# Kernel optimization log

Hardware: AMD Instinct MI355X
Metric: run time of the kernel (lower is better)

The kernel has to match this reference:

```python
import jax, jax.numpy as jnp
import numpy as np

HEADS = 8
DIM_HEAD = 64


def setup_inputs() -> dict:
    key = jax.random.key(0)
    ks = jax.random.split(key, 5)
    dim = 512
    dim_inner = HEADS * DIM_HEAD
    return {
        "fmap": jax.random.normal(ks[0], (8, dim, 32, 32), dtype=jnp.float32),
        "gamma": jnp.ones((dim,), dtype=jnp.float32),
        "wq": jax.random.normal(ks[1], (dim_inner, dim), dtype=jnp.float32) * 0.05,
        "wv": jax.random.normal(ks[2], (dim_inner, dim), dtype=jnp.float32) * 0.05,
        "null_kv": jax.random.normal(ks[3], (2, HEADS, DIM_HEAD), dtype=jnp.float32),
        "wo": jax.random.normal(ks[4], (dim, dim_inner), dtype=jnp.float32) * 0.05,
    }


def reference(fmap, gamma, wq, wv, null_kv, wo):
    b, c, H, W = fmap.shape
    h, d = HEADS, DIM_HEAD
    n = H * W
    scale = d ** (-0.5)

    # ChannelRMSNorm: F.normalize over channel dim * sqrt(dim) * gamma
    l2 = jnp.sqrt(jnp.sum(fmap * fmap, axis=1, keepdims=True))
    x = fmap / jnp.maximum(l2, 1e-12) * (c ** 0.5) * gamma[None, :, None, None]

    # 1x1 convs as channel matmuls -> [b, h, n, d]
    def proj(w):
        t = jnp.einsum('bcxy,oc->boxy', x, w)          # [b, h*d, H, W]
        return t.reshape(b, h, d, n).transpose(0, 1, 3, 2)  # [b, h, n, d]

    q = proj(wq)
    v = proj(wv)
    k = q  # dot_product=False -> to_k is None, k = q

    # prepend null kv token
    nk = jnp.broadcast_to(null_kv[0][None, :, None, :], (b, h, 1, d))
    nv = jnp.broadcast_to(null_kv[1][None, :, None, :], (b, h, 1, d))
    k = jnp.concatenate([nk, k], axis=2)  # [b, h, n+1, d]
    v = jnp.concatenate([nv, v], axis=2)

    # negative squared L2 distance score: -(|q|^2 + |k|^2 - 2 q.k)
    q_sq = jnp.sum(q * q, axis=-1)  # [b, h, n]
    k_sq = jnp.sum(k * k, axis=-1)  # [b, h, n+1]
    qk = jnp.einsum('bhid,bhjd->bhij', q, k)
    sim = -(q_sq[..., :, None] + k_sq[..., None, :] - 2.0 * qk) * scale

    attn = jax.nn.softmax(sim, axis=-1)
    out = jnp.einsum('bhij,bhjd->bhid', attn, v)  # [b, h, n, d]

    out = out.transpose(0, 1, 3, 2).reshape(b, h * d, H, W)
    return jnp.einsum('boxy,co->bcxy', out, wo)
```

## Files before the change

### kernel.cpp

```cpp
#include <hip/hip_runtime.h>
#include <hip/hip_bf16.h>

#define DEV static __device__ __forceinline__

typedef __bf16 bf16x8 __attribute__((ext_vector_type(8)));
typedef float f32x4 __attribute__((ext_vector_type(4)));
typedef float f32x16 __attribute__((ext_vector_type(16)));
typedef unsigned u32x4 __attribute__((ext_vector_type(4)));
typedef unsigned short u16x8 __attribute__((ext_vector_type(8)));
typedef unsigned short u16x4 __attribute__((ext_vector_type(4)));

DEV unsigned short f2bf(float f) {
  unsigned u = __builtin_bit_cast(unsigned, f);
  u += 0x7fffu + ((u >> 16) & 1u);
  return (unsigned short)(u >> 16);
}
DEV float bf2f(unsigned short s) {
  return __builtin_bit_cast(float, (unsigned)s << 16);
}
DEV f32x4 mfma16(bf16x8 a, bf16x8 b, f32x4 c) {
  return __builtin_amdgcn_mfma_f32_16x16x32_bf16(a, b, c, 0, 0, 0);
}
DEV f32x16 mfma32(bf16x8 a, bf16x8 b, f32x16 c) {
  return __builtin_amdgcn_mfma_f32_32x32x16_bf16(a, b, c, 0, 0, 0);
}
DEV bf16x8 ld8(const unsigned short* p) {
  return __builtin_bit_cast(bf16x8, *(const u16x8*)p);
}
DEV void gload16(const unsigned short* g, unsigned short* l) {
  auto* g1 = reinterpret_cast<const __attribute__((address_space(1))) unsigned int*>(
      reinterpret_cast<uintptr_t>(g));
  auto* l3 = reinterpret_cast<__attribute__((address_space(3))) unsigned int*>(
      reinterpret_cast<uintptr_t>(l));
  __builtin_amdgcn_global_load_lds(g1, l3, 16, 0, 0);
}

__global__ __launch_bounds__(256) void prep_k(const float* __restrict__ fmap,
                                              const float* __restrict__ gamma,
                                              const float* __restrict__ wq,
                                              const float* __restrict__ wv,
                                              const float* __restrict__ wo,
                                              unsigned short* __restrict__ xt,
                                              unsigned short* __restrict__ wqb,
                                              unsigned short* __restrict__ wvb,
                                              unsigned short* __restrict__ wob) {
  int bid = blockIdx.x, tid = threadIdx.x;
  if (bid >= 256) {
    int t4 = bid - 256;
    int g = t4 >> 5;
    const float* src = (g == 0) ? wq : (g == 1) ? wv : wo;
    unsigned short* dst = (g == 0) ? wqb : (g == 1) ? wvb : wob;
    int base = (t4 & 31) * 1024 + tid;
    const float4* s = (const float4*)src;
#pragma unroll
    for (int i = 0; i < 4; ++i) {
      int idx = base + i * 256;
      float4 a = s[idx * 2], b = s[idx * 2 + 1];
      u16x8 o;
      o[0] = f2bf(a.x); o[1] = f2bf(a.y); o[2] = f2bf(a.z); o[3] = f2bf(a.w);
      o[4] = f2bf(b.x); o[5] = f2bf(b.y); o[6] = f2bf(b.z); o[7] = f2bf(b.w);
      ((u16x8*)dst)[idx] = o;
    }
    return;
  }
  __shared__ float slab[512][33];
  __shared__ float red[8][32];
  __shared__ float rn_l[32];
  __shared__ float gl[512];
  int b = bid >> 5, n0 = (bid & 31) * 32;
  gl[tid] = gamma[tid];
  gl[tid + 256] = gamma[tid + 256];
  int n_l = tid & 31, cg = tid >> 5;
  const float* p = fmap + ((size_t)(b * 512 + cg * 64)) * 1024 + n0 + n_l;
  float s = 0.f;
#pragma unroll 8
  for (int i = 0; i < 64; ++i) {
    float v = p[i * 1024];
    slab[cg * 64 + i][n_l] = v;
    s += v * v;
  }
  red[cg][n_l] = s;
  __syncthreads();
  if (tid < 32) {
    float ts = 0.f;
#pragma unroll
    for (int k = 0; k < 8; ++k) ts += red[k][tid];
    rn_l[tid] = 22.62741699796952f / fmaxf(sqrtf(ts), 1e-12f);
  }
  __syncthreads();
  int nn = tid >> 3, cc = tid & 7;
  float sc = rn_l[nn];
#pragma unroll
  for (int c0 = 0; c0 < 512; c0 += 64) {
    u16x8 o;
#pragma unroll
    for (int e = 0; e < 8; ++e) {
      int c = c0 + cc * 8 + e;
      o[e] = f2bf(slab[c][nn] * sc * gl[c]);
    }
    *(u16x8*)(xt + ((size_t)(b * 1024 + n0 + nn)) * 512 + c0 + cc * 8) = o;
  }
}

__global__ __launch_bounds__(512) void gemm_qv_k(const unsigned short* __restrict__ A,
                                                 const unsigned short* __restrict__ wqb,
                                                 const unsigned short* __restrict__ wvb,
                                                 const float* __restrict__ nkv,
                                                 unsigned short* __restrict__ QF,
                                                 unsigned short* __restrict__ VF,
                                                 float* __restrict__ qsqs,
                                                 float* __restrict__ p0g) {
  __shared__ unsigned short a_lds[128 * 64];
  __shared__ unsigned short bq_lds[128 * 64];
  __shared__ unsigned short bv_lds[128 * 64];
  int tid = threadIdx.x, lane = tid & 63, wid = tid >> 6;
  int isV = wid >> 2, gw = wid & 3;
  int wr = gw >> 1, wc = gw & 1;
  int m0 = blockIdx.y * 128, n0 = blockIdx.x * 128;
  int srow = (lane >> 3);
  int scol = ((lane & 7) ^ ((lane >> 3) & 7)) * 8;
  f32x4 acc[4][4] = {};
  for (int kt = 0; kt < 512; kt += 64) {
    int il0 = wid * 2;
#pragma unroll
    for (int i = 0; i < 2; ++i) {
      int il = il0 + i;
      gload16(A + (size_t)(m0 + il * 8 + srow) * 512 + kt + scol, &a_lds[il * 512]);
      gload16(wqb + (size_t)(n0 + il * 8 + srow) * 512 + kt + scol, &bq_lds[il * 512]);
      gload16(wvb + (size_t)(n0 + il * 8 + srow) * 512 + kt + scol, &bv_lds[il * 512]);
    }
    __syncthreads();
    const unsigned short* bl = isV ? bv_lds : bq_lds;
#pragma unroll
    for (int ks = 0; ks < 2; ++ks) {
      int c = ks * 4 + (lane >> 4);
      int cs = (c ^ (lane & 7)) * 8;
      bf16x8 af[4], bfr[4];
#pragma unroll
      for (int rt = 0; rt < 4; ++rt)
        af[rt] = ld8(&a_lds[(wr * 64 + rt * 16 + (lane & 15)) * 64 + cs]);
#pragma unroll
      for (int ct = 0; ct < 4; ++ct)
        bfr[ct] = ld8(&bl[(wc * 64 + ct * 16 + (lane & 15)) * 64 + cs]);
#pragma unroll
      for (int rt = 0; rt < 4; ++rt)
#pragma unroll
        for (int ct = 0; ct < 4; ++ct)
          acc[rt][ct] = mfma16(af[rt], bfr[ct], acc[rt][ct]);
    }
    __syncthreads();
  }
  if (!isV) {
    const float COEF = 0.18033688011112042f;
    int head = blockIdx.x * 2 + wc;
    const float* nk = nkv + head * 64;
    float nk_own[4], nks = 0.f;
#pragma unroll
    for (int ct = 0; ct < 4; ++ct) {
      nk_own[ct] = nk[ct * 16 + (lane & 15)];
      nks += nk_own[ct] * nk_own[ct];
    }
    nks += __shfl_xor(nks, 1); nks += __shfl_xor(nks, 2);
    nks += __shfl_xor(nks, 4); nks += __shfl_xor(nks, 8);
#pragma unroll
    for (int rt = 0; rt < 4; ++rt)
#pragma unroll
      for (int r = 0; r < 4; ++r) {
        float qs = 0.f, dot = 0.f;
        unsigned short qr[4];
#pragma unroll
        for (int ct = 0; ct < 4; ++ct) {
          unsigned short us = f2bf(acc[rt][ct][r]);
          qr[ct] = us;
          float v = bf2f(us);
          qs += v * v;
          dot += v * nk_own[ct];
        }
        int n = m0 + wr * 64 + rt * 16 + (lane >> 4) * 4 + r;
        int bb = n >> 10, nl = n & 1023;
        int bh = bb * 8 + head;
        size_t fidx = (size_t)(bh * 32 + (nl >> 5)) * 2048 + (nl & 31) * 16 + (lane & 15);
#pragma unroll
        for (int ct = 0; ct < 4; ++ct) QF[fidx + ct * 512] = qr[ct];
        qs += __shfl_xor(qs, 1); qs += __shfl_xor(qs, 2);
        qs += __shfl_xor(qs, 4); qs += __shfl_xor(qs, 8);
        dot += __shfl_xor(dot, 1); dot += __shfl_xor(dot, 2);
        dot += __shfl_xor(dot, 4); dot += __shfl_xor(dot, 8);
        if ((lane & 15) == 0) {
          qsqs[bh * 1024 + nl] = qs * COEF;
          p0g[bh * 1024 + nl] = __builtin_amdgcn_exp2f((2.f * dot - nks) * COEF);
        }
      }
  } else {
#pragma unroll
    for (int rt = 0; rt < 4; ++rt)
#pragma unroll
      for (int ct = 0; ct < 4; ++ct) {
        int nb = m0 + wr * 64 + rt * 16 + (lane >> 4) * 4;
        int o = n0 + wc * 64 + ct * 16 + (lane & 15);
        int b = nb >> 10, j = nb & 1023;
        int h = o >> 6, d = o & 63;
        int bh = b * 8 + h;
        size_t idx = (size_t)(bh * 32 + (j >> 5)) * 2048 + ((j >> 4) & 1) * 1024 + (d >> 5) * 512 +
                     (d & 31) * 16 + (j & 15);
        u16x4 pk;
#pragma unroll
        for (int r = 0; r < 4; ++r) pk[r] = f2bf(acc[rt][ct][r]);
        *(u16x4*)(VF + idx) = pk;
      }
  }
}

__global__ __launch_bounds__(256) void gemm_o_k(const unsigned short* __restrict__ A,
                                                const unsigned short* __restrict__ Bt,
                                                float* __restrict__ Cp) {
  __shared__ unsigned short a_lds[64 * 64];
  __shared__ unsigned short b_lds[128 * 64];
  int bid = blockIdx.x;
  int y = (bid >> 3) & 7;
  int x = (bid & 7) + ((bid >> 6) << 3);
  int m0 = y * 64, n0 = x * 128;
  int tid = threadIdx.x, lane = tid & 63, wid = tid >> 6;
  int wr = wid >> 1, wc = wid & 1;
  int srow = (lane >> 3);
  int scol = ((lane & 7) ^ ((lane >> 3) & 7)) * 8;
  f32x4 acc[2][4] = {};
  for (int kt = 0; kt < 512; kt += 64) {
#pragma unroll
    for (int i = 0; i < 2; ++i) {
      int il = wid * 2 + i;
      gload16(A + (size_t)(m0 + il * 8 + srow) * 512 + kt + scol, &a_lds[il * 512]);
    }
#pragma unroll
    for (int i = 0; i < 4; ++i) {
      int il = wid * 4 + i;
      gload16(Bt + (size_t)(n0 + il * 8 + srow) * 512 + kt + scol, &b_lds[il * 512]);
    }
    __syncthreads();
#pragma unroll
    for (int ks = 0; ks < 2; ++ks) {
      int c = ks * 4 + (lane >> 4);
      int cs = (c ^ (lane & 7)) * 8;
      bf16x8 af[2], bfr[4];
#pragma unroll
      for (int rt = 0; rt < 2; ++rt)
        af[rt] = ld8(&a_lds[(wr * 32 + rt * 16 + (lane & 15)) * 64 + cs]);
#pragma unroll
      for (int ct = 0; ct < 4; ++ct)
        bfr[ct] = ld8(&b_lds[(wc * 64 + ct * 16 + (lane & 15)) * 64 + cs]);
#pragma unroll
      for (int rt = 0; rt < 2; ++rt)
#pragma unroll
        for (int ct = 0; ct < 4; ++ct)
          acc[rt][ct] = mfma16(af[rt], bfr[ct], acc[rt][ct]);
    }
    __syncthreads();
  }
  int bb = n0 >> 10;
#pragma unroll
  for (int rt = 0; rt < 2; ++rt)
#pragma unroll
    for (int ct = 0; ct < 4; ++ct)
#pragma unroll
      for (int r = 0; r < 4; ++r) {
        int row = m0 + wr * 32 + rt * 16 + (lane >> 4) * 4 + r;
        int col = (n0 & 1023) + wc * 64 + ct * 16 + (lane & 15);
        Cp[((size_t)(bb * 512 + row)) * 1024 + col] = acc[rt][ct][r];
      }
}

__global__ __launch_bounds__(512) void attn_k(const unsigned short* __restrict__ QF,
                                              const unsigned short* __restrict__ VF,
                                              const float* __restrict__ qsqs,
                                              const float* __restrict__ p0g,
                                              const float* __restrict__ nkv,
                                              unsigned short* __restrict__ att) {
  const float C2 = 0.36067376022224085f;
  int bid = blockIdx.x;
  int s0 = bid >> 3;
  int bh = ((bid & 7) << 3) | (s0 & 7);
  int qt = s0 >> 3;
  int b = bh >> 3, h = bh & 7;
  int n0 = qt * 128;
  int tid = threadIdx.x, lane = tid & 63, wid = tid >> 6;
  int wq = wid & 3, jg = wid >> 2;
  int l31 = lane & 31, hi = lane >> 5;

  __shared__ float ob_l[32][4][64];
  __shared__ float dsb[4][32];
  __shared__ float p0_l[128];
  __shared__ float nv_l[64];
  __shared__ float dn_l[4][32];

  if (tid < 128) p0_l[tid] = p0g[bh * 1024 + n0 + tid];
  else if (tid < 192) nv_l[tid - 128] = nkv[512 + h * 64 + (tid - 128)];
  __syncthreads();

  bf16x8 qf[4];
  const unsigned short* qfp = QF + (size_t)(bh * 32 + qt * 4 + wq) * 2048 + l31 * 16 + hi * 8;
#pragma unroll
  for (int ks = 0; ks < 4; ++ks)
    qf[ks] = ld8(qfp + ks * 512);

  f32x16 oacc[2];
#pragma unroll
  for (int dh = 0; dh < 2; ++dh)
#pragma unroll
    for (int r = 0; r < 16; ++r) {
      int row = (r & 3) + 8 * (r >> 2) + 4 * hi;
      oacc[dh][r] = (jg == 0) ? p0_l[wq * 32 + row] * nv_l[dh * 32 + l31] : 0.f;
    }

  f32x4 dsum4 = {0.f, 0.f, 0.f, 0.f};
  const unsigned short* kbase = QF + (size_t)bh * 65536 + l31 * 16 + hi * 8;
  const unsigned short* vbase = VF + (size_t)bh * 65536 + l31 * 16 + hi * 8;
  const float* ksb = qsqs + bh * 1024 + 4 * hi;

  bf16x8 kfA[4], kfB[4], vfA[2][2], vfB[2][2];
  f32x4 ksqA[4], ksqB[4];

#define LOADT(S, JT)                                                        \
  {                                                                         \
    const unsigned short* kp_ = kbase + (JT) * 2048;                        \
    kf##S[0] = ld8(kp_);        kf##S[1] = ld8(kp_ + 512);                  \
    kf##S[2] = ld8(kp_ + 1024); kf##S[3] = ld8(kp_ + 1536);                 \
    const unsigned short* vp_ = vbase + (JT) * 2048;                        \
    vf##S[0][0] = ld8(vp_);        vf##S[0][1] = ld8(vp_ + 1024);           \
    vf##S[1][0] = ld8(vp_ + 512);  vf##S[1][1] = ld8(vp_ + 1536);           \
    const float* kq_ = ksb + (JT) * 32;                                     \
    ksq##S[0] = *(const f32x4*)(kq_);      ksq##S[1] = *(const f32x4*)(kq_ + 8);  \
    ksq##S[2] = *(const f32x4*)(kq_ + 16); ksq##S[3] = *(const f32x4*)(kq_ + 24); \
  }

#define COMPT(S)                                                            \
  {                                                                         \
    f32x16 sacc = {};                                                       \
    __builtin_amdgcn_s_setprio(1);                                          \
    sacc = mfma32(kf##S[0], qf[0], sacc);                                   \
    sacc = mfma32(kf##S[1], qf[1], sacc);                                   \
    sacc = mfma32(kf##S[2], qf[2], sacc);                                   \
    sacc = mfma32(kf##S[3], qf[3], sacc);                                   \
    __builtin_amdgcn_s_setprio(0);                                          \
    float p[16];                                                            \
    _Pragma("unroll")                                                       \
    for (int r = 0; r < 16; ++r) {                                          \
      p[r] = __builtin_amdgcn_exp2f(sacc[r] * C2 - ksq##S[r >> 2][r & 3]);  \
      dsum4[r & 3] += p[r];                                                 \
    }                                                                       \
    unsigned w[4][2];                                                       \
    _Pragma("unroll")                                                       \
    for (int m = 0; m < 4; ++m) {                                           \
      asm("v_cvt_pk_bf16_f32 %0, %1, %2" : "=v"(w[m][0]) : "v"(p[4 * m]), "v"(p[4 * m + 1]));     \
      asm("v_cvt_pk_bf16_f32 %0, %1, %2" : "=v"(w[m][1]) : "v"(p[4 * m + 2]), "v"(p[4 * m + 3])); \
    }                                                                       \
    __builtin_amdgcn_s_setprio(1);                                          \
    _Pragma("unroll")                                                       \
    for (int sj = 0; sj < 2; ++sj) {                                        \
      unsigned a0 = w[2 * sj][0], b0 = w[2 * sj + 1][0];                    \
      unsigned a1 = w[2 * sj][1], b1 = w[2 * sj + 1][1];                    \
      asm("v_permlane32_swap_b32 %0, %1" : "+v"(a0), "+v"(b0));             \
      asm("v_permlane32_swap_b32 %0, %1" : "+v"(a1), "+v"(b1));             \
      u32x4 pw; pw[0] = a0; pw[1] = a1; pw[2] = b0; pw[3] = b1;             \
      bf16x8 pa = __builtin_bit_cast(bf16x8, pw);                           \
      oacc[0] = mfma32(pa, vf##S[0][sj], oacc[0]);                          \
      oacc[1] = mfma32(pa, vf##S[1][sj], oacc[1]);                          \
    }                                                                       \
    __builtin_amdgcn_s_setprio(0);                                          \
  }

  int jb = jg * 16;
  LOADT(A, jb)
#pragma unroll 1
  for (int s = 0; s < 7; ++s) {
    LOADT(B, jb + 2 * s + 1)
    COMPT(A)
    LOADT(A, jb + 2 * s + 2)
    COMPT(B)
  }
  LOADT(B, jb + 15)
  COMPT(A)
  COMPT(B)

  float dsum = (dsum4[0] + dsum4[1]) + (dsum4[2] + dsum4[3]);
  dsum += __shfl_xor(dsum, 32);

  if (jg == 1) {
#pragma unroll
    for (int dh = 0; dh < 2; ++dh)
#pragma unroll
      for (int r = 0; r < 16; ++r)
        ob_l[dh * 16 + r][wq][lane] = oacc[dh][r];
    if (hi == 0) dsb[wq][l31] = dsum;
  }
  __syncthreads();
  if (jg == 0) {
#pragma unroll
    for (int dh = 0; dh < 2; ++dh)
#pragma unroll
      for (int r = 0; r < 16; ++r)
        oacc[dh][r] += ob_l[dh * 16 + r][wq][lane];
    dsum += dsb[wq][l31] + p0_l[wq * 32 + l31];
    float rden = 1.0f / dsum;
    if (hi == 0) dn_l[wq][l31] = rden;
  }
  __syncthreads();

  if (jg == 0) {
#pragma unroll
    for (int dh = 0; dh < 2; ++dh)
#pragma unroll
      for (int r = 0; r < 16; ++r) {
        int row = (r & 3) + 8 * (r >> 2) + 4 * hi;
        float o = oacc[dh][r] * dn_l[wq][row];
        att[((size_t)(b * 1024 + n0 + wq * 32 + row)) * 512 + h * 64 + dh * 32 + l31] = f2bf(o);
      }
  }
}

extern "C" void kernel_launch(void* const* d_in, const int* in_sizes, int n_in,
                              void* d_out, int out_size, void* d_ws, size_t ws_size,
                              hipStream_t stream) {
  const float* fmap = (const float*)d_in[0];
  const float* gamma = (const float*)d_in[1];
  const float* wq = (const float*)d_in[2];
  const float* wv = (const float*)d_in[3];
  const float* nkv = (const float*)d_in[4];
  const float* wo = (const float*)d_in[5];
  float* out = (float*)d_out;

  const size_t M4 = (size_t)8192 * 512;
  unsigned short* x_t = (unsigned short*)d_ws;
  unsigned short* QF  = x_t + M4;
  unsigned short* VF  = QF + M4;
  unsigned short* att = VF + M4;
  unsigned short* wqb = att + M4;
  unsigned short* wvb = wqb + (size_t)512 * 512;
  unsigned short* wob = wvb + (size_t)512 * 512;
  float* qsqs = (float*)(wob + (size_t)512 * 512);
  float* p0g  = qsqs + 65536;

  prep_k<<<352, 256, 0, stream>>>(fmap, gamma, wq, wv, wo, x_t, wqb, wvb, wob);
  gemm_qv_k<<<dim3(4, 64), 512, 0, stream>>>(x_t, wqb, wvb, nkv, QF, VF, qsqs, p0g);
  attn_k<<<512, 512, 0, stream>>>(QF, VF, qsqs, p0g, nkv, att);
  gemm_o_k<<<512, 256, 0, stream>>>(wob, att, out);
}
```

Baseline: 69.84 us.

## Double-buffer LDS tiles in projection GEMMs and split QK MFMA accumulator chains

Both the QV projection GEMM and the output GEMM now keep two LDS buffers, so the global-to-LDS loads for the next K tile are issued before computing on the current one. This is meant to hide global load latency behind the MFMA work, at the cost of twice the shared memory, which may lower occupancy. In the attention kernel, the four dependent QK MFMAs are split into two independent accumulators that are summed before the exp. This shortens the MFMA dependency chain at the cost of one extra add per element.

```diff
diff --git a/kernel.cpp b/kernel.cpp
--- a/kernel.cpp
+++ b/kernel.cpp
@@ -110,9 +110,9 @@
                                                  unsigned short* __restrict__ VF,
                                                  float* __restrict__ qsqs,
                                                  float* __restrict__ p0g) {
-  __shared__ unsigned short a_lds[128 * 64];
-  __shared__ unsigned short bq_lds[128 * 64];
-  __shared__ unsigned short bv_lds[128 * 64];
+  __shared__ unsigned short a_lds[2][128 * 64];
+  __shared__ unsigned short bq_lds[2][128 * 64];
+  __shared__ unsigned short bv_lds[2][128 * 64];
   int tid = threadIdx.x, lane = tid & 63, wid = tid >> 6;
   int isV = wid >> 2, gw = wid & 3;
   int wr = gw >> 1, wc = gw & 1;
@@ -120,17 +120,28 @@
   int srow = (lane >> 3);
   int scol = ((lane & 7) ^ ((lane >> 3) & 7)) * 8;
   f32x4 acc[4][4] = {};
-  for (int kt = 0; kt < 512; kt += 64) {
-    int il0 = wid * 2;
-#pragma unroll
-    for (int i = 0; i < 2; ++i) {
-      int il = il0 + i;
-      gload16(A + (size_t)(m0 + il * 8 + srow) * 512 + kt + scol, &a_lds[il * 512]);
-      gload16(wqb + (size_t)(n0 + il * 8 + srow) * 512 + kt + scol, &bq_lds[il * 512]);
-      gload16(wvb + (size_t)(n0 + il * 8 + srow) * 512 + kt + scol, &bv_lds[il * 512]);
-    }
-    __syncthreads();
-    const unsigned short* bl = isV ? bv_lds : bq_lds;
+
+#define QV_STAGE(BUF, KT)                                                          \
+  {                                                                                \
+    int il0 = wid * 2;                                                             \
+    _Pragma("unroll")                                                              \
+    for (int i = 0; i < 2; ++i) {                                                  \
+      int il = il0 + i;                                                            \
+      gload16(A + (size_t)(m0 + il * 8 + srow) * 512 + (KT) + scol, &a_lds[BUF][il * 512]);   \
+      gload16(wqb + (size_t)(n0 + il * 8 + srow) * 512 + (KT) + scol, &bq_lds[BUF][il * 512]); \
+      gload16(wvb + (size_t)(n0 + il * 8 + srow) * 512 + (KT) + scol, &bv_lds[BUF][il * 512]); \
+    }                                                                              \
+  }
+
+  QV_STAGE(0, 0)
+  asm volatile("s_waitcnt vmcnt(0)" ::: "memory");
+  __syncthreads();
+  int cur = 0;
+#pragma unroll 1
+  for (int t = 0; t < 8; ++t) {
+    if (t < 7) QV_STAGE(cur ^ 1, (t + 1) * 64)
+    const unsigned short* al = &a_lds[cur][0];
+    const unsigned short* bl = isV ? &bv_lds[cur][0] : &bq_lds[cur][0];
 #pragma unroll
     for (int ks = 0; ks < 2; ++ks) {
       int c = ks * 4 + (lane >> 4);
@@ -138,7 +149,7 @@
       bf16x8 af[4], bfr[4];
 #pragma unroll
       for (int rt = 0; rt < 4; ++rt)
-        af[rt] = ld8(&a_lds[(wr * 64 + rt * 16 + (lane & 15)) * 64 + cs]);
+        af[rt] = ld8(&al[(wr * 64 + rt * 16 + (lane & 15)) * 64 + cs]);
 #pragma unroll
       for (int ct = 0; ct < 4; ++ct)
         bfr[ct] = ld8(&bl[(wc * 64 + ct * 16 + (lane & 15)) * 64 + cs]);
@@ -148,7 +159,9 @@
         for (int ct = 0; ct < 4; ++ct)
           acc[rt][ct] = mfma16(af[rt], bfr[ct], acc[rt][ct]);
     }
+    asm volatile("s_waitcnt vmcnt(0)" ::: "memory");
     __syncthreads();
+    cur ^= 1;
   }
   if (!isV) {
     const float COEF = 0.18033688011112042f;
@@ -214,8 +227,8 @@
 __global__ __launch_bounds__(256) void gemm_o_k(const unsigned short* __restrict__ A,
                                                 const unsigned short* __restrict__ Bt,
                                                 float* __restrict__ Cp) {
-  __shared__ unsigned short a_lds[64 * 64];
-  __shared__ unsigned short b_lds[128 * 64];
+  __shared__ unsigned short a_lds[2][64 * 64];
+  __shared__ unsigned short b_lds[2][128 * 64];
   int bid = blockIdx.x;
   int y = (bid >> 3) & 7;
   int x = (bid & 7) + ((bid >> 6) << 3);
@@ -225,18 +238,30 @@
   int srow = (lane >> 3);
   int scol = ((lane & 7) ^ ((lane >> 3) & 7)) * 8;
   f32x4 acc[2][4] = {};
-  for (int kt = 0; kt < 512; kt += 64) {
-#pragma unroll
-    for (int i = 0; i < 2; ++i) {
-      int il = wid * 2 + i;
-      gload16(A + (size_t)(m0 + il * 8 + srow) * 512 + kt + scol, &a_lds[il * 512]);
-    }
-#pragma unroll
-    for (int i = 0; i < 4; ++i) {
-      int il = wid * 4 + i;
-      gload16(Bt + (size_t)(n0 + il * 8 + srow) * 512 + kt + scol, &b_lds[il * 512]);
-    }
-    __syncthreads();
+
+#define O_STAGE(BUF, KT)                                                           \
+  {                                                                                \
+    _Pragma("unroll")                                                              \
+    for (int i = 0; i < 2; ++i) {                                                  \
+      int il = wid * 2 + i;                                                        \
+      gload16(A + (size_t)(m0 + il * 8 + srow) * 512 + (KT) + scol, &a_lds[BUF][il * 512]);    \
+    }                                                                              \
+    _Pragma("unroll")                                                              \
+    for (int i = 0; i < 4; ++i) {                                                  \
+      int il = wid * 4 + i;                                                        \
+      gload16(Bt + (size_t)(n0 + il * 8 + srow) * 512 + (KT) + scol, &b_lds[BUF][il * 512]);   \
+    }                                                                              \
+  }
+
+  O_STAGE(0, 0)
+  asm volatile("s_waitcnt vmcnt(0)" ::: "memory");
+  __syncthreads();
+  int cur = 0;
+#pragma unroll 1
+  for (int t = 0; t < 8; ++t) {
+    if (t < 7) O_STAGE(cur ^ 1, (t + 1) * 64)
+    const unsigned short* al = &a_lds[cur][0];
+    const unsigned short* bl = &b_lds[cur][0];
 #pragma unroll
     for (int ks = 0; ks < 2; ++ks) {
       int c = ks * 4 + (lane >> 4);
@@ -244,17 +269,19 @@
       bf16x8 af[2], bfr[4];
 #pragma unroll
       for (int rt = 0; rt < 2; ++rt)
-        af[rt] = ld8(&a_lds[(wr * 32 + rt * 16 + (lane & 15)) * 64 + cs]);
+        af[rt] = ld8(&al[(wr * 32 + rt * 16 + (lane & 15)) * 64 + cs]);
 #pragma unroll
       for (int ct = 0; ct < 4; ++ct)
-        bfr[ct] = ld8(&b_lds[(wc * 64 + ct * 16 + (lane & 15)) * 64 + cs]);
+        bfr[ct] = ld8(&bl[(wc * 64 + ct * 16 + (lane & 15)) * 64 + cs]);
 #pragma unroll
       for (int rt = 0; rt < 2; ++rt)
 #pragma unroll
         for (int ct = 0; ct < 4; ++ct)
           acc[rt][ct] = mfma16(af[rt], bfr[ct], acc[rt][ct]);
     }
+    asm volatile("s_waitcnt vmcnt(0)" ::: "memory");
     __syncthreads();
+    cur ^= 1;
   }
   int bb = n0 >> 10;
 #pragma unroll
@@ -334,17 +361,17 @@
 
 #define COMPT(S)                                                            \
   {                                                                         \
-    f32x16 sacc = {};                                                       \
+    f32x16 sa = {}, sb = {};                                                \
     __builtin_amdgcn_s_setprio(1);                                          \
-    sacc = mfma32(kf##S[0], qf[0], sacc);                                   \
-    sacc = mfma32(kf##S[1], qf[1], sacc);                                   \
-    sacc = mfma32(kf##S[2], qf[2], sacc);                                   \
-    sacc = mfma32(kf##S[3], qf[3], sacc);                                   \
+    sa = mfma32(kf##S[0], qf[0], sa);                                       \
+    sb = mfma32(kf##S[1], qf[1], sb);                                       \
+    sa = mfma32(kf##S[2], qf[2], sa);                                       \
+    sb = mfma32(kf##S[3], qf[3], sb);                                       \
     __builtin_amdgcn_s_setprio(0);                                          \
     float p[16];                                                            \
     _Pragma("unroll")                                                       \
     for (int r = 0; r < 16; ++r) {                                          \
-      p[r] = __builtin_amdgcn_exp2f(sacc[r] * C2 - ksq##S[r >> 2][r & 3]);  \
+      p[r] = __builtin_amdgcn_exp2f((sa[r] + sb[r]) * C2 - ksq##S[r >> 2][r & 3]);  \
       dsum4[r & 3] += p[r];                                                 \
     }                                                                       \
     unsigned w[4][2];                                                       \
```

Measured after the change: 67.33 us. 1.04x faster.
